# Kernel tuning notes

Measured on AMD Instinct MI355X. Metric: run time of the kernel, lower is better.

## Reference

```python
import jax, jax.numpy as jnp
import numpy as np

B, T, H, W = 1, 8, 48, 48
EMBED, HEADS = 512, 8
HD = EMBED // HEADS          # 64
KS = 3                       # spatial neighborhood kernel
ROT = HD // 3                # 21 -> 2*(21//2)=20 rotary dims per axis, 60 total
MAX_FREQ = 256.0
EPS = 1e-6


def _rms_norm(x, w):
    return x * jax.lax.rsqrt(jnp.mean(x * x, axis=-1, keepdims=True) + EPS) * w


def _axis_freqs(L, base):
    # freqs_for='pixel': positions in [-1, 1], freqs = linspace(1, max_freq/2)*pi
    pos = jnp.linspace(-1.0, 1.0, L)
    f = pos[:, None] * base[None, :]          # (L, ROT//2)
    return jnp.repeat(f, 2, axis=-1)          # (L, 2*(ROT//2)) interleaved pairs


def _axial_freqs(t, h, w):
    base = jnp.linspace(1.0, MAX_FREQ / 2.0, ROT // 2) * jnp.pi
    ft, fh, fw = _axis_freqs(t, base), _axis_freqs(h, base), _axis_freqs(w, base)
    d = ft.shape[-1]
    ft = jnp.broadcast_to(ft[:, None, None, :], (t, h, w, d))
    fh = jnp.broadcast_to(fh[None, :, None, :], (t, h, w, d))
    fw = jnp.broadcast_to(fw[None, None, :, :], (t, h, w, d))
    return jnp.concatenate([ft, fh, fw], axis=-1)  # (t, h, w, 3*d)


def _rotate_half(x):
    x1, x2 = x[..., ::2], x[..., 1::2]
    return jnp.stack((-x2, x1), axis=-1).reshape(x.shape)


def _apply_rope(freqs, x):
    r = freqs.shape[-1]
    xr, xt = x[..., :r], x[..., r:]
    xr = xr * jnp.cos(freqs) + _rotate_half(xr) * jnp.sin(freqs)
    return jnp.concatenate([xr, xt], axis=-1)


def reference(x, w_qkv, w_out, qnorm_w, knorm_w):
    b, t, h, w, c = x.shape
    # fused QKV: per-head contiguous [q|k|v] chunk of size 3*HD (matches
    # rearrange '(heads head_dim)' with head_dim = 3*HD, then tensor_split(3, -1))
    qkv = (x @ w_qkv.T).reshape(b, t, h, w, HEADS, 3 * HD)
    q, k, v = qkv[..., :HD], qkv[..., HD:2 * HD], qkv[..., 2 * HD:]
    q = _rms_norm(q, qnorm_w)
    k = _rms_norm(k, knorm_w)
    freqs = _axial_freqs(t, h, w)[:, :, :, None, :]  # broadcast over heads
    q = _apply_rope(freqs, q)
    k = _apply_rope(freqs, k)
    # neighborhood attention: full along t, clamped KSxKS window over (h, w)
    ih = jnp.clip(jnp.arange(h) - KS // 2, 0, h - KS)[:, None] + jnp.arange(KS)
    iw = jnp.clip(jnp.arange(w) - KS // 2, 0, w - KS)[:, None] + jnp.arange(KS)
    IH = ih[:, :, None, None]  # (h, KS, 1, 1)
    IW = iw[None, None, :, :]  # (1, 1, w, KS)
    kw = k[:, :, IH, IW]       # (b, t, h, KS, w, KS, heads, HD)
    vw = v[:, :, IH, IW]
    scores = jnp.einsum('btxynd,bsxiyjnd->bntxysij', q, kw) * (HD ** -0.5)
    attn = jax.nn.softmax(scores.reshape(b, HEADS, t, h, w, -1), axis=-1)
    attn = attn.reshape(scores.shape)
    out = jnp.einsum('bntxysij,bsxiyjnd->btxynd', attn, vw)
    out = out.reshape(b, t, h, w, c)
    return out @ w_out.T


def setup_inputs():
    key = jax.random.key(0)
    k1, k2, k3 = jax.random.split(key, 3)
    x = jax.random.normal(k1, (B, T, H, W, EMBED), jnp.float32)
    w_qkv = jax.random.normal(k2, (3 * EMBED, EMBED), jnp.float32) * 0.02
    w_out = jax.random.normal(k3, (EMBED, EMBED), jnp.float32) * 0.02
    qnorm_w = jnp.ones((HD,), jnp.float32)
    knorm_w = jnp.ones((HD,), jnp.float32)
    return dict(x=x, w_qkv=w_qkv, w_out=w_out, qnorm_w=qnorm_w, knorm_w=knorm_w)
```

## Files before the change

### kernel.cpp

```cpp
#include <hip/hip_runtime.h>
#include <hip/hip_bf16.h>
#include <math.h>

#define TOK 18432
#define EMB 512
#define NH 8
#define HD_ 64
#define HH 48
#define WW 48

typedef __attribute__((ext_vector_type(8))) __bf16 bf16x8;
typedef __attribute__((ext_vector_type(4))) float  f32x4;
typedef __attribute__((ext_vector_type(8))) unsigned short u16x8;

__device__ __forceinline__ ushort f2bf(float x) {
    __hip_bfloat16 b = __float2bfloat16(x);
    return *(ushort*)&b;
}
__device__ __forceinline__ float bf2f(ushort u) {
    __hip_bfloat16 b = *(__hip_bfloat16*)&u;
    return __bfloat162float(b);
}

__device__ __forceinline__ void gload16(const void* g, void* l) {
    __builtin_amdgcn_global_load_lds((const __attribute__((address_space(1))) void*)g,
                                     (__attribute__((address_space(3))) void*)l,
                                     16, 0, 0);
}

__device__ __forceinline__ f32x4 mfma_bf16(bf16x8 a, bf16x8 b, f32x4 c) {
    return __builtin_amdgcn_mfma_f32_16x16x32_bf16(a, b, c, 0, 0, 0);
}

__global__ void fill_tabs(float2* __restrict__ tabs) {
    int idx = blockIdx.x * 256 + threadIdx.x;
    if (idx >= 104 * 10) return;
    int row = idx / 10, j = idx % 10;
    float base = fmaf((float)j, 127.0f / 9.0f, 1.0f) * 3.14159265358979323846f;
    float pos;
    if (row < 8)       pos = fmaf((float)row,        2.0f / 7.0f,  -1.0f);
    else if (row < 56) pos = fmaf((float)(row - 8),  2.0f / 47.0f, -1.0f);
    else               pos = fmaf((float)(row - 56), 2.0f / 47.0f, -1.0f);
    float f = pos * base;
    tabs[idx] = make_float2(cosf(f), sinf(f));
}

__global__ __launch_bounds__(256) void conv_hi(const float* __restrict__ src,
                                               ushort* __restrict__ dst, int n4) {
    int i = blockIdx.x * 256 + threadIdx.x;
    if (i >= n4) return;
    float4 v = ((const float4*)src)[i];
    ushort4 h = {f2bf(v.x), f2bf(v.y), f2bf(v.z), f2bf(v.w)};
    ((ushort4*)dst)[i] = h;
}

__global__ __launch_bounds__(256) void gemm_qkv(const ushort* __restrict__ Ah,
                                                const ushort* __restrict__ Bh,
                                                const float2* __restrict__ tabs,
                                                const float* __restrict__ qnw,
                                                const float* __restrict__ knw,
                                                ushort* __restrict__ qbf,
                                                ushort* __restrict__ kbf,
                                                ushort* __restrict__ vbf) {
    const int K = 512, nM = 12;
    __shared__ __align__(16) char smem[32768];
#define AS_(b) ((ushort*)(smem + (b) * 8192))
#define BS_(b) ((ushort*)(smem + 16384 + (b) * 8192))
    int nwg = gridDim.x;
    int bid = blockIdx.x;
    int cpx = nwg >> 3;
    int swz = (bid & 7) * cpx + (bid >> 3);
    int bm = (swz % nM) * 128, bn = (swz / nM) * 128;
    int tid = threadIdx.x;
    int lane = tid & 63, wave = tid >> 6;
    int wr = wave >> 1, wc = wave & 1;
    int fr = lane & 15, kg = lane >> 4;

    f32x4 acc[4][4];
#pragma unroll
    for (int m = 0; m < 4; ++m)
#pragma unroll
        for (int n = 0; n < 4; ++n) acc[m][n] = (f32x4){0.f, 0.f, 0.f, 0.f};

    auto stage = [&](int buf, int k0) {
#pragma unroll
        for (int it = 0; it < 2; ++it) {
            int f = it * 256 + tid;
            int row = f >> 2, ch = f & 3;
            int sl = ch ^ ((row >> 1) & 3);
            gload16(Ah + (size_t)(bm + row) * K + k0 + sl * 8, AS_(buf) + f * 8);
            gload16(Bh + (size_t)(bn + row) * K + k0 + sl * 8, BS_(buf) + f * 8);
        }
    };

    int nt = K >> 5;
    stage(0, 0);
    __syncthreads();
    int cur = 0;
    int ksw = (kg ^ ((fr >> 1) & 3)) * 8;
    for (int t = 0; t < nt; ++t) {
        if (t + 1 < nt) stage(cur ^ 1, (t + 1) << 5);
        bf16x8 bh[4];
#pragma unroll
        for (int n = 0; n < 4; ++n)
            bh[n] = *(const bf16x8*)&BS_(cur)[(wc * 64 + n * 16 + fr) * 32 + ksw];
#pragma unroll
        for (int m = 0; m < 4; ++m) {
            bf16x8 ah = *(const bf16x8*)&AS_(cur)[(wr * 64 + m * 16 + fr) * 32 + ksw];
#pragma unroll
            for (int n = 0; n < 4; ++n)
                acc[m][n] = mfma_bf16(ah, bh[n], acc[m][n]);
        }
        __syncthreads();
        cur ^= 1;
    }

    int g = (bm >> 6) + wr;
    int type = g % 3;
    int h = g / 3;
    ushort* obuf = (type == 0) ? qbf : (type == 1) ? kbf : vbf;
    float qsc = (type == 0) ? 0.125f : 1.0f;
    float4 wv[4];
    if (type < 2) {
        const float* wptr = type ? knw : qnw;
#pragma unroll
        for (int m = 0; m < 4; ++m)
            wv[m] = *(const float4*)&wptr[m * 16 + kg * 4];
    }
    char* tb = smem + wave * 5120;
    size_t obase = (size_t)h * TOK + bn + wc * 64;

#pragma unroll
    for (int hp = 0; hp < 2; ++hp) {
#pragma unroll
        for (int nn = 0; nn < 2; ++nn) {
            int n = hp * 2 + nn;
            int tk = bn + wc * 64 + n * 16 + fr;
            if (type == 2) {
#pragma unroll
                for (int m = 0; m < 4; ++m) {
                    ushort4 pk = {f2bf(acc[m][n][0]), f2bf(acc[m][n][1]),
                                  f2bf(acc[m][n][2]), f2bf(acc[m][n][3])};
                    *(ushort4*)(tb + (nn * 16 + fr) * 160 + (m * 16 + kg * 4) * 2) = pk;
                }
            } else {
                float s = 0.f;
#pragma unroll
                for (int m = 0; m < 4; ++m)
#pragma unroll
                    for (int i = 0; i < 4; ++i)
                        s = fmaf(acc[m][n][i], acc[m][n][i], s);
                s += __shfl_xor(s, 16);
                s += __shfl_xor(s, 32);
                float inv = rsqrtf(s * (1.0f / 64.0f) + 1e-6f);
                int t = tk / (HH * WW);
                int rem = tk % (HH * WW);
                int xx = rem / WW, yy = rem % WW;
#pragma unroll
                for (int m = 0; m < 4; ++m) {
                    float r[4];
                    const float* wm = (const float*)&wv[m];
#pragma unroll
                    for (int u = 0; u < 2; ++u) {
                        int dc0 = m * 16 + kg * 4 + 2 * u;
                        float xn0 = acc[m][n][2 * u]     * inv * wm[2 * u];
                        float xn1 = acc[m][n][2 * u + 1] * inv * wm[2 * u + 1];
                        if (dc0 < 60) {
                            int p = dc0 >> 1;
                            int tr = (p < 10) ? t * 10 + p
                                   : (p < 20) ? (8 + xx) * 10 + (p - 10)
                                              : (56 + yy) * 10 + (p - 20);
                            float2 cs = tabs[tr];
                            r[2 * u]     = fmaf(xn0, cs.x, -xn1 * cs.y);
                            r[2 * u + 1] = fmaf(xn1, cs.x,  xn0 * cs.y);
                        } else {
                            r[2 * u] = xn0;
                            r[2 * u + 1] = xn1;
                        }
                    }
                    ushort4 pk = {f2bf(r[0] * qsc), f2bf(r[1] * qsc),
                                  f2bf(r[2] * qsc), f2bf(r[3] * qsc)};
                    *(ushort4*)(tb + (nn * 16 + fr) * 160 + (m * 16 + kg * 4) * 2) = pk;
                }
            }
        }
#pragma unroll
        for (int j = 0; j < 4; ++j) {
            int row = j * 8 + (lane >> 3);
            int c16 = (lane & 7) * 16;
            u16x8 v = *(const u16x8*)(tb + row * 160 + c16);
            size_t tok = obase + hp * 32 + row;
            *(u16x8*)(obuf + tok * 64 + (lane & 7) * 8) = v;
        }
    }
#undef AS_
#undef BS_
}

__global__ __launch_bounds__(256) void gemm_out(const ushort* __restrict__ Ah,
                                                const ushort* __restrict__ Bh,
                                                float* __restrict__ C) {
    const int N = 512, K = 512, nbx = 4;
    __shared__ __align__(16) ushort As[2][128 * 32];
    __shared__ __align__(16) ushort Bs[2][128 * 32];
    int nwg = gridDim.x;
    int bid = blockIdx.x;
    int cpx = nwg >> 3;
    int swz = (bid & 7) * cpx + (bid >> 3);
    int bm = (swz / nbx) * 128, bn = (swz % nbx) * 128;
    int tid = threadIdx.x;
    int lane = tid & 63, wave = tid >> 6;
    int wr = wave >> 1, wc = wave & 1;
    int fr = lane & 15, kg = lane >> 4;

    f32x4 acc[4][4];
#pragma unroll
    for (int m = 0; m < 4; ++m)
#pragma unroll
        for (int n = 0; n < 4; ++n) acc[m][n] = (f32x4){0.f, 0.f, 0.f, 0.f};

    auto stage = [&](int buf, int k0) {
#pragma unroll
        for (int it = 0; it < 2; ++it) {
            int f = it * 256 + tid;
            int row = f >> 2, ch = f & 3;
            int sl = ch ^ ((row >> 1) & 3);
            gload16(Ah + (size_t)(bm + row) * K + k0 + sl * 8, &As[buf][f * 8]);
            gload16(Bh + (size_t)(bn + row) * K + k0 + sl * 8, &Bs[buf][f * 8]);
        }
    };

    int nt = K >> 5;
    stage(0, 0);
    __syncthreads();
    int cur = 0;
    int ksw = (kg ^ ((fr >> 1) & 3)) * 8;
    for (int t = 0; t < nt; ++t) {
        if (t + 1 < nt) stage(cur ^ 1, (t + 1) << 5);
        bf16x8 bh[4];
#pragma unroll
        for (int n = 0; n < 4; ++n)
            bh[n] = *(const bf16x8*)&Bs[cur][(wc * 64 + n * 16 + fr) * 32 + ksw];
#pragma unroll
        for (int m = 0; m < 4; ++m) {
            bf16x8 ah = *(const bf16x8*)&As[cur][(wr * 64 + m * 16 + fr) * 32 + ksw];
#pragma unroll
            for (int n = 0; n < 4; ++n)
                acc[m][n] = mfma_bf16(ah, bh[n], acc[m][n]);
        }
        __syncthreads();
        cur ^= 1;
    }
#pragma unroll
    for (int m = 0; m < 4; ++m) {
        int row0 = bm + wr * 64 + m * 16 + kg * 4;
#pragma unroll
        for (int n = 0; n < 4; ++n) {
            int col = bn + wc * 64 + n * 16 + fr;
#pragma unroll
            for (int i = 0; i < 4; ++i)
                C[(size_t)(row0 + i) * N + col] = acc[m][n][i];
        }
    }
}

__global__ __launch_bounds__(256) void attn_mfma(const ushort* __restrict__ qbf,
                                                 const ushort* __restrict__ kbf,
                                                 const ushort* __restrict__ vbf,
                                                 ushort* __restrict__ ohi) {
    __shared__ __align__(16) char smem[45056];
    constexpr int Q_OFF = 0;
    constexpr int K_OFF = 4096;
    constexpr int V_OFF = 20480;
    constexpr int P_OFF = 36864;

    int patch = blockIdx.x, head = blockIdx.y;
    int bi = patch / 24, bj = patch % 24;
    int x0 = bi * 2, y0 = bj * 2;
    int ubx = min(max(x0 - 1, 0), 44), uby = min(max(y0 - 1, 0), 44);
    int tid = threadIdx.x, lane = tid & 63, w = tid >> 6;
    int fr = lane & 15, kg = lane >> 4;
    size_t hbase = (size_t)head * TOK;

    {
        int f = tid;
        int row = f >> 3, sp = f & 7, sl = sp ^ (row & 7);
        int t = row >> 2, px = (row >> 1) & 1, py = row & 1;
        size_t tok = ((size_t)(t * HH + x0 + px)) * WW + (y0 + py);
        gload16(qbf + (hbase + tok) * 64 + sl * 8, smem + Q_OFF + f * 16);
    }
#pragma unroll
    for (int it = 0; it < 4; ++it) {
        int f = it * 256 + tid;
        int row = f >> 3, sp = f & 7, sl = sp ^ (row & 7);
        int s = row >> 4, ki = (row >> 2) & 3, kj = row & 3;
        size_t tok = ((size_t)(s * HH + ubx + ki)) * WW + (uby + kj);
        gload16(kbf + (hbase + tok) * 64 + sl * 8, smem + K_OFF + f * 16);
    }
#pragma unroll
    for (int it = 0; it < 2; ++it) {
        int u = it * 256 + tid;
        int sk = u >> 4, dg = u & 15;
        int s = sk >> 2, ki = sk & 3;
        ushort4 rv[4];
#pragma unroll
        for (int kj = 0; kj < 4; ++kj) {
            size_t tok = ((size_t)(s * HH + ubx + ki)) * WW + (uby + kj);
            rv[kj] = *(const ushort4*)(vbf + (hbase + tok) * 64 + dg * 4);
        }
        const ushort* rr = (const ushort*)rv;
#pragma unroll
        for (int dd = 0; dd < 4; ++dd) {
            int d = dg * 4 + dd;
            ushort4 val = {rr[dd], rr[4 + dd], rr[8 + dd], rr[12 + dd]};
            *(ushort4*)(smem + V_OFF + d * 256 + ((sk * 2 * 4) ^ ((d & 7) << 4))) = val;
        }
    }
    __syncthreads();

    if (w < 2) {
        int q = w * 16 + fr;
        bf16x8 qb[2];
#pragma unroll
        for (int ks = 0; ks < 2; ++ks)
            qb[ks] = *(const bf16x8*)(smem + Q_OFF + q * 128 +
                                      ((ks * 64 + kg * 16) ^ ((fr & 7) << 4)));
        f32x4 sc[8];
#pragma unroll
        for (int m = 0; m < 8; ++m) sc[m] = (f32x4){0.f, 0.f, 0.f, 0.f};
#pragma unroll
        for (int m = 0; m < 8; ++m)
#pragma unroll
            for (int ks = 0; ks < 2; ++ks) {
                bf16x8 a = *(const bf16x8*)(smem + K_OFF + (m * 16 + fr) * 128 +
                                            ((ks * 64 + kg * 16) ^ ((fr & 7) << 4)));
                sc[m] = mfma_bf16(a, qb[ks], sc[m]);
            }
        int xq = x0 + ((q >> 1) & 1), yq = y0 + (q & 1);
        int lox = min(max(xq - 1, 0), 45) - ubx;
        int loy = min(max(yq - 1, 0), 45) - uby;
        bool vki = ((unsigned)(kg - lox)) <= 2u;
        float mx = -1e30f;
        if (vki) {
#pragma unroll
            for (int m = 0; m < 8; ++m)
#pragma unroll
                for (int i = 0; i < 4; ++i)
                    if (((unsigned)(i - loy)) <= 2u) mx = fmaxf(mx, sc[m][i]);
        }
        mx = fmaxf(mx, __shfl_xor(mx, 16));
        mx = fmaxf(mx, __shfl_xor(mx, 32));
        float sum = 0.f;
#pragma unroll
        for (int m = 0; m < 8; ++m)
#pragma unroll
            for (int i = 0; i < 4; ++i) {
                bool v = vki && (((unsigned)(i - loy)) <= 2u);
                float e = v ? __expf(sc[m][i] - mx) : 0.f;
                sc[m][i] = e;
                sum += e;
            }
        sum += __shfl_xor(sum, 16);
        sum += __shfl_xor(sum, 32);
        float inv = 1.0f / sum;
#pragma unroll
        for (int m = 0; m < 8; ++m) {
            ushort4 pk = {f2bf(sc[m][0] * inv), f2bf(sc[m][1] * inv),
                          f2bf(sc[m][2] * inv), f2bf(sc[m][3] * inv)};
            *(ushort4*)(smem + P_OFF + q * 256 +
                        ((m * 32 + kg * 8) ^ ((q & 7) << 4))) = pk;
        }
    }
    __syncthreads();

    f32x4 ov[2];
    ov[0] = (f32x4){0.f, 0.f, 0.f, 0.f};
    ov[1] = (f32x4){0.f, 0.f, 0.f, 0.f};
#pragma unroll
    for (int kb = 0; kb < 4; ++kb) {
        bf16x8 a = *(const bf16x8*)(smem + V_OFF + (w * 16 + fr) * 256 +
                                    ((kb * 64 + kg * 16) ^ ((fr & 7) << 4)));
#pragma unroll
        for (int nt2 = 0; nt2 < 2; ++nt2) {
            bf16x8 b = *(const bf16x8*)(smem + P_OFF + (nt2 * 16 + fr) * 256 +
                                        ((kb * 64 + kg * 16) ^ ((fr & 7) << 4)));
            ov[nt2] = mfma_bf16(a, b, ov[nt2]);
        }
    }
#pragma unroll
    for (int nt2 = 0; nt2 < 2; ++nt2) {
        int q = nt2 * 16 + fr;
        int t = q >> 2, px = (q >> 1) & 1, py = q & 1;
        size_t tok = ((size_t)(t * HH + x0 + px)) * WW + (y0 + py);
        size_t ob = tok * 512 + head * 64 + w * 16 + kg * 4;
        ushort4 hv = {f2bf(ov[nt2][0]), f2bf(ov[nt2][1]),
                      f2bf(ov[nt2][2]), f2bf(ov[nt2][3])};
        *(ushort4*)&ohi[ob] = hv;
    }
}

extern "C" void kernel_launch(void* const* d_in, const int* in_sizes, int n_in,
                              void* d_out, int out_size, void* d_ws, size_t ws_size,
                              hipStream_t stream) {
    const float* x     = (const float*)d_in[0];
    const float* w_qkv = (const float*)d_in[1];
    const float* w_out = (const float*)d_in[2];
    const float* qnw   = (const float*)d_in[3];
    const float* knw   = (const float*)d_in[4];
    float* out = (float*)d_out;
    char*  ws  = (char*)d_ws;

    const size_t TABS_B = 16384;
    const size_t WQ_B   = (size_t)1536 * 512 * 2;
    const size_t WO_B   = (size_t)512 * 512 * 2;

    float2* tabs = (float2*)ws;
    ushort* wqhi = (ushort*)(ws + TABS_B);
    ushort* wohi = wqhi + (size_t)1536 * 512;
    ushort* qbf  = (ushort*)(ws + TABS_B + WQ_B + WO_B);
    ushort* kbf  = qbf + (size_t)TOK * 512;
    ushort* vbf  = kbf + (size_t)TOK * 512;
    ushort* ohi  = vbf + (size_t)TOK * 512;

    ushort* xhi = (ushort*)d_out;

    fill_tabs<<<5, 256, 0, stream>>>(tabs);
    conv_hi<<<(TOK * 512 / 4 + 255) / 256, 256, 0, stream>>>(x, xhi, TOK * 512 / 4);
    conv_hi<<<(1536 * 512 / 4 + 255) / 256, 256, 0, stream>>>(w_qkv, wqhi, 1536 * 512 / 4);
    conv_hi<<<(512 * 512 / 4 + 255) / 256, 256, 0, stream>>>(w_out, wohi, 512 * 512 / 4);

    gemm_qkv<<<(1536 / 128) * (TOK / 128), 256, 0, stream>>>(
        wqhi, xhi, tabs, qnw, knw, qbf, kbf, vbf);
    attn_mfma<<<dim3(576, NH), 256, 0, stream>>>(qbf, kbf, vbf, ohi);
    gemm_out<<<(TOK / 128) * (512 / 128), 256, 0, stream>>>(ohi, wohi, out);
}
```

Baseline: 117.2 us.

## Fuse x fp32-to-bf16 conversion into QKV GEMM staging and merge init kernels

The separate pass that converted x to bf16 is removed. The QKV GEMM now loads fp32 x tiles straight into registers, converts them, and writes them to LDS while the MFMAs run, instead of using a direct global-to-LDS copy of pre-converted data. The two weight conversions and the rope table fill are merged into one launch. This saves a full read and write of x plus several launches, but each x tile is now re-read in fp32 by all 12 N-blocks, which doubles that traffic, and the B staging goes through registers.

```diff
diff --git a/kernel.cpp b/kernel.cpp
--- a/kernel.cpp
+++ b/kernel.cpp
@@ -32,30 +32,35 @@
     return __builtin_amdgcn_mfma_f32_16x16x32_bf16(a, b, c, 0, 0, 0);
 }
 
-__global__ void fill_tabs(float2* __restrict__ tabs) {
-    int idx = blockIdx.x * 256 + threadIdx.x;
-    if (idx >= 104 * 10) return;
-    int row = idx / 10, j = idx % 10;
-    float base = fmaf((float)j, 127.0f / 9.0f, 1.0f) * 3.14159265358979323846f;
-    float pos;
-    if (row < 8)       pos = fmaf((float)row,        2.0f / 7.0f,  -1.0f);
-    else if (row < 56) pos = fmaf((float)(row - 8),  2.0f / 47.0f, -1.0f);
-    else               pos = fmaf((float)(row - 56), 2.0f / 47.0f, -1.0f);
-    float f = pos * base;
-    tabs[idx] = make_float2(cosf(f), sinf(f));
-}
-
-__global__ __launch_bounds__(256) void conv_hi(const float* __restrict__ src,
-                                               ushort* __restrict__ dst, int n4) {
-    int i = blockIdx.x * 256 + threadIdx.x;
-    if (i >= n4) return;
-    float4 v = ((const float4*)src)[i];
-    ushort4 h = {f2bf(v.x), f2bf(v.y), f2bf(v.z), f2bf(v.w)};
-    ((ushort4*)dst)[i] = h;
+__global__ __launch_bounds__(256) void init_misc(const float* __restrict__ wq,
+                                                 ushort* __restrict__ wqhi,
+                                                 const float* __restrict__ wo,
+                                                 ushort* __restrict__ wohi,
+                                                 float2* __restrict__ tabs) {
+    int b = blockIdx.x;
+    if (b < 1024) {
+        const float* src = (b < 768) ? wq : wo;
+        ushort* dst = (b < 768) ? wqhi : wohi;
+        int i = (b < 768 ? b : b - 768) * 256 + threadIdx.x;
+        float4 v = ((const float4*)src)[i];
+        ushort4 h = {f2bf(v.x), f2bf(v.y), f2bf(v.z), f2bf(v.w)};
+        ((ushort4*)dst)[i] = h;
+    } else {
+        int idx = (b - 1024) * 256 + threadIdx.x;
+        if (idx >= 104 * 10) return;
+        int row = idx / 10, j = idx % 10;
+        float base = fmaf((float)j, 127.0f / 9.0f, 1.0f) * 3.14159265358979323846f;
+        float pos;
+        if (row < 8)       pos = fmaf((float)row,        2.0f / 7.0f,  -1.0f);
+        else if (row < 56) pos = fmaf((float)(row - 8),  2.0f / 47.0f, -1.0f);
+        else               pos = fmaf((float)(row - 56), 2.0f / 47.0f, -1.0f);
+        float f = pos * base;
+        tabs[idx] = make_float2(cosf(f), sinf(f));
+    }
 }
 
 __global__ __launch_bounds__(256) void gemm_qkv(const ushort* __restrict__ Ah,
-                                                const ushort* __restrict__ Bh,
+                                                const float* __restrict__ Bx,
                                                 const float2* __restrict__ tabs,
                                                 const float* __restrict__ qnw,
                                                 const float* __restrict__ knw,
@@ -82,24 +87,46 @@
 #pragma unroll
         for (int n = 0; n < 4; ++n) acc[m][n] = (f32x4){0.f, 0.f, 0.f, 0.f};
 
-    auto stage = [&](int buf, int k0) {
-#pragma unroll
-        for (int it = 0; it < 2; ++it) {
-            int f = it * 256 + tid;
-            int row = f >> 2, ch = f & 3;
-            int sl = ch ^ ((row >> 1) & 3);
-            gload16(Ah + (size_t)(bm + row) * K + k0 + sl * 8, AS_(buf) + f * 8);
-            gload16(Bh + (size_t)(bn + row) * K + k0 + sl * 8, BS_(buf) + f * 8);
-        }
+    int rowA0 = tid >> 2,           chA0 = tid & 3;
+    int slA0 = chA0 ^ ((rowA0 >> 1) & 3);
+    int rowA1 = (256 + tid) >> 2,   chA1 = (256 + tid) & 3;
+    int slA1 = chA1 ^ ((rowA1 >> 1) & 3);
+    const float* bsrc0 = Bx + (size_t)(bn + rowA0) * K + slA0 * 8;
+    const float* bsrc1 = Bx + (size_t)(bn + rowA1) * K + slA1 * 8;
+
+    auto issueA = [&](int buf, int k0) {
+        gload16(Ah + (size_t)(bm + rowA0) * K + k0 + slA0 * 8, AS_(buf) + tid * 8);
+        gload16(Ah + (size_t)(bm + rowA1) * K + k0 + slA1 * 8, AS_(buf) + (256 + tid) * 8);
     };
 
     int nt = K >> 5;
-    stage(0, 0);
+    issueA(0, 0);
+    {
+        float4 b00 = *(const float4*)(bsrc0);
+        float4 b01 = *(const float4*)(bsrc0 + 4);
+        float4 b10 = *(const float4*)(bsrc1);
+        float4 b11 = *(const float4*)(bsrc1 + 4);
+        u16x8 w0 = {f2bf(b00.x), f2bf(b00.y), f2bf(b00.z), f2bf(b00.w),
+                    f2bf(b01.x), f2bf(b01.y), f2bf(b01.z), f2bf(b01.w)};
+        u16x8 w1 = {f2bf(b10.x), f2bf(b10.y), f2bf(b10.z), f2bf(b10.w),
+                    f2bf(b11.x), f2bf(b11.y), f2bf(b11.z), f2bf(b11.w)};
+        *(u16x8*)(BS_(0) + tid * 8) = w0;
+        *(u16x8*)(BS_(0) + (256 + tid) * 8) = w1;
+    }
     __syncthreads();
+
     int cur = 0;
     int ksw = (kg ^ ((fr >> 1) & 3)) * 8;
     for (int t = 0; t < nt; ++t) {
-        if (t + 1 < nt) stage(cur ^ 1, (t + 1) << 5);
+        float4 b00, b01, b10, b11;
+        if (t + 1 < nt) {
+            int k0n = (t + 1) << 5;
+            issueA(cur ^ 1, k0n);
+            b00 = *(const float4*)(bsrc0 + k0n);
+            b01 = *(const float4*)(bsrc0 + k0n + 4);
+            b10 = *(const float4*)(bsrc1 + k0n);
+            b11 = *(const float4*)(bsrc1 + k0n + 4);
+        }
         bf16x8 bh[4];
 #pragma unroll
         for (int n = 0; n < 4; ++n)
@@ -110,6 +137,14 @@
 #pragma unroll
             for (int n = 0; n < 4; ++n)
                 acc[m][n] = mfma_bf16(ah, bh[n], acc[m][n]);
+        }
+        if (t + 1 < nt) {
+            u16x8 w0 = {f2bf(b00.x), f2bf(b00.y), f2bf(b00.z), f2bf(b00.w),
+                        f2bf(b01.x), f2bf(b01.y), f2bf(b01.z), f2bf(b01.w)};
+            u16x8 w1 = {f2bf(b10.x), f2bf(b10.y), f2bf(b10.z), f2bf(b10.w),
+                        f2bf(b11.x), f2bf(b11.y), f2bf(b11.z), f2bf(b11.w)};
+            *(u16x8*)(BS_(cur ^ 1) + tid * 8) = w0;
+            *(u16x8*)(BS_(cur ^ 1) + (256 + tid) * 8) = w1;
         }
         __syncthreads();
         cur ^= 1;
@@ -313,7 +348,7 @@
         for (int dd = 0; dd < 4; ++dd) {
             int d = dg * 4 + dd;
             ushort4 val = {rr[dd], rr[4 + dd], rr[8 + dd], rr[12 + dd]};
-            *(ushort4*)(smem + V_OFF + d * 256 + ((sk * 2 * 4) ^ ((d & 7) << 4))) = val;
+            *(ushort4*)(smem + V_OFF + d * 256 + ((sk * 8) ^ ((d & 7) << 4))) = val;
         }
     }
     __syncthreads();
@@ -422,15 +457,10 @@
     ushort* vbf  = kbf + (size_t)TOK * 512;
     ushort* ohi  = vbf + (size_t)TOK * 512;
 
-    ushort* xhi = (ushort*)d_out;
-
-    fill_tabs<<<5, 256, 0, stream>>>(tabs);
-    conv_hi<<<(TOK * 512 / 4 + 255) / 256, 256, 0, stream>>>(x, xhi, TOK * 512 / 4);
-    conv_hi<<<(1536 * 512 / 4 + 255) / 256, 256, 0, stream>>>(w_qkv, wqhi, 1536 * 512 / 4);
-    conv_hi<<<(512 * 512 / 4 + 255) / 256, 256, 0, stream>>>(w_out, wohi, 512 * 512 / 4);
+    init_misc<<<1029, 256, 0, stream>>>(w_qkv, wqhi, w_out, wohi, tabs);
 
     gemm_qkv<<<(1536 / 128) * (TOK / 128), 256, 0, stream>>>(
-        wqhi, xhi, tabs, qnw, knw, qbf, kbf, vbf);
+        wqhi, x, tabs, qnw, knw, qbf, kbf, vbf);
     attn_mfma<<<dim3(576, NH), 256, 0, stream>>>(qbf, kbf, vbf, ohi);
     gemm_out<<<(TOK / 128) * (512 / 128), 256, 0, stream>>>(ohi, wohi, out);
 }
```

Result: faster. 113.1 us (-3.5%).

## Fuse x fp32-to-bf16 conversion into QKV GEMM and merge init kernels

Applied to the files above, without the earlier changes.

The separate pass that converts the activation tensor x to bf16 is removed. The QKV GEMM now stages fp32 x tiles directly into LDS with a swizzled layout and converts them to bf16 while loading MFMA fragments. The weight conversions and the rotary table fill are merged into a single launch. This saves a full read and write of x and several launches. In exchange it doubles the LDS footprint and B-tile load traffic per GEMM block, and it repeats the conversion work for each of the 12 M-tiles that read the same x tile.

```diff
diff --git a/kernel.cpp b/kernel.cpp
--- a/kernel.cpp
+++ b/kernel.cpp
@@ -32,30 +32,35 @@
     return __builtin_amdgcn_mfma_f32_16x16x32_bf16(a, b, c, 0, 0, 0);
 }
 
-__global__ void fill_tabs(float2* __restrict__ tabs) {
-    int idx = blockIdx.x * 256 + threadIdx.x;
-    if (idx >= 104 * 10) return;
-    int row = idx / 10, j = idx % 10;
-    float base = fmaf((float)j, 127.0f / 9.0f, 1.0f) * 3.14159265358979323846f;
-    float pos;
-    if (row < 8)       pos = fmaf((float)row,        2.0f / 7.0f,  -1.0f);
-    else if (row < 56) pos = fmaf((float)(row - 8),  2.0f / 47.0f, -1.0f);
-    else               pos = fmaf((float)(row - 56), 2.0f / 47.0f, -1.0f);
-    float f = pos * base;
-    tabs[idx] = make_float2(cosf(f), sinf(f));
-}
-
-__global__ __launch_bounds__(256) void conv_hi(const float* __restrict__ src,
-                                               ushort* __restrict__ dst, int n4) {
-    int i = blockIdx.x * 256 + threadIdx.x;
-    if (i >= n4) return;
-    float4 v = ((const float4*)src)[i];
-    ushort4 h = {f2bf(v.x), f2bf(v.y), f2bf(v.z), f2bf(v.w)};
-    ((ushort4*)dst)[i] = h;
+__global__ __launch_bounds__(256) void init_misc(const float* __restrict__ wq,
+                                                 ushort* __restrict__ wqhi,
+                                                 const float* __restrict__ wo,
+                                                 ushort* __restrict__ wohi,
+                                                 float2* __restrict__ tabs) {
+    int b = blockIdx.x;
+    if (b < 1024) {
+        const float* src = (b < 768) ? wq : wo;
+        ushort* dst = (b < 768) ? wqhi : wohi;
+        int i = (b < 768 ? b : b - 768) * 256 + threadIdx.x;
+        float4 v = ((const float4*)src)[i];
+        ushort4 h = {f2bf(v.x), f2bf(v.y), f2bf(v.z), f2bf(v.w)};
+        ((ushort4*)dst)[i] = h;
+    } else {
+        int idx = (b - 1024) * 256 + threadIdx.x;
+        if (idx >= 104 * 10) return;
+        int row = idx / 10, j = idx % 10;
+        float base = fmaf((float)j, 127.0f / 9.0f, 1.0f) * 3.14159265358979323846f;
+        float pos;
+        if (row < 8)       pos = fmaf((float)row,        2.0f / 7.0f,  -1.0f);
+        else if (row < 56) pos = fmaf((float)(row - 8),  2.0f / 47.0f, -1.0f);
+        else               pos = fmaf((float)(row - 56), 2.0f / 47.0f, -1.0f);
+        float f = pos * base;
+        tabs[idx] = make_float2(cosf(f), sinf(f));
+    }
 }
 
 __global__ __launch_bounds__(256) void gemm_qkv(const ushort* __restrict__ Ah,
-                                                const ushort* __restrict__ Bh,
+                                                const float* __restrict__ Bx,
                                                 const float2* __restrict__ tabs,
                                                 const float* __restrict__ qnw,
                                                 const float* __restrict__ knw,
@@ -63,9 +68,9 @@
                                                 ushort* __restrict__ kbf,
                                                 ushort* __restrict__ vbf) {
     const int K = 512, nM = 12;
-    __shared__ __align__(16) char smem[32768];
-#define AS_(b) ((ushort*)(smem + (b) * 8192))
-#define BS_(b) ((ushort*)(smem + 16384 + (b) * 8192))
+    __shared__ __align__(16) char smem[49152];
+#define AS_(b)  ((ushort*)(smem + (b) * 8192))
+#define BSF_(b) ((float*)(smem + 16384 + (b) * 16384))
     int nwg = gridDim.x;
     int bid = blockIdx.x;
     int cpx = nwg >> 3;
@@ -89,7 +94,13 @@
             int row = f >> 2, ch = f & 3;
             int sl = ch ^ ((row >> 1) & 3);
             gload16(Ah + (size_t)(bm + row) * K + k0 + sl * 8, AS_(buf) + f * 8);
-            gload16(Bh + (size_t)(bn + row) * K + k0 + sl * 8, BS_(buf) + f * 8);
+        }
+#pragma unroll
+        for (int it = 0; it < 4; ++it) {
+            int f = it * 256 + tid;
+            int row = f >> 3, ch = f & 7;
+            int sl = ch ^ (row & 7);
+            gload16(Bx + (size_t)(bn + row) * K + k0 + sl * 4, BSF_(buf) + f * 4);
         }
     };
 
@@ -97,16 +108,24 @@
     stage(0, 0);
     __syncthreads();
     int cur = 0;
-    int ksw = (kg ^ ((fr >> 1) & 3)) * 8;
+    int aw = (kg ^ ((fr >> 1) & 3)) * 8;
+    int r7 = fr & 7;
     for (int t = 0; t < nt; ++t) {
         if (t + 1 < nt) stage(cur ^ 1, (t + 1) << 5);
+        const float* BF = BSF_(cur);
         bf16x8 bh[4];
 #pragma unroll
-        for (int n = 0; n < 4; ++n)
-            bh[n] = *(const bf16x8*)&BS_(cur)[(wc * 64 + n * 16 + fr) * 32 + ksw];
+        for (int n = 0; n < 4; ++n) {
+            int R = wc * 64 + n * 16 + fr;
+            f32x4 lo = *(const f32x4*)(BF + R * 32 + (((kg * 2)     ^ r7) << 2));
+            f32x4 hi = *(const f32x4*)(BF + R * 32 + (((kg * 2 + 1) ^ r7) << 2));
+            u16x8 tw = {f2bf(lo[0]), f2bf(lo[1]), f2bf(lo[2]), f2bf(lo[3]),
+                        f2bf(hi[0]), f2bf(hi[1]), f2bf(hi[2]), f2bf(hi[3])};
+            bh[n] = *(bf16x8*)&tw;
+        }
 #pragma unroll
         for (int m = 0; m < 4; ++m) {
-            bf16x8 ah = *(const bf16x8*)&AS_(cur)[(wr * 64 + m * 16 + fr) * 32 + ksw];
+            bf16x8 ah = *(const bf16x8*)&AS_(cur)[(wr * 64 + m * 16 + fr) * 32 + aw];
 #pragma unroll
             for (int n = 0; n < 4; ++n)
                 acc[m][n] = mfma_bf16(ah, bh[n], acc[m][n]);
@@ -194,7 +213,7 @@
         }
     }
 #undef AS_
-#undef BS_
+#undef BSF_
 }
 
 __global__ __launch_bounds__(256) void gemm_out(const ushort* __restrict__ Ah,
@@ -313,7 +332,7 @@
         for (int dd = 0; dd < 4; ++dd) {
             int d = dg * 4 + dd;
             ushort4 val = {rr[dd], rr[4 + dd], rr[8 + dd], rr[12 + dd]};
-            *(ushort4*)(smem + V_OFF + d * 256 + ((sk * 2 * 4) ^ ((d & 7) << 4))) = val;
+            *(ushort4*)(smem + V_OFF + d * 256 + ((sk * 8) ^ ((d & 7) << 4))) = val;
         }
     }
     __syncthreads();
@@ -422,15 +441,10 @@
     ushort* vbf  = kbf + (size_t)TOK * 512;
     ushort* ohi  = vbf + (size_t)TOK * 512;
 
-    ushort* xhi = (ushort*)d_out;
-
-    fill_tabs<<<5, 256, 0, stream>>>(tabs);
-    conv_hi<<<(TOK * 512 / 4 + 255) / 256, 256, 0, stream>>>(x, xhi, TOK * 512 / 4);
-    conv_hi<<<(1536 * 512 / 4 + 255) / 256, 256, 0, stream>>>(w_qkv, wqhi, 1536 * 512 / 4);
-    conv_hi<<<(512 * 512 / 4 + 255) / 256, 256, 0, stream>>>(w_out, wohi, 512 * 512 / 4);
+    init_misc<<<1029, 256, 0, stream>>>(w_qkv, wqhi, w_out, wohi, tabs);
 
     gemm_qkv<<<(1536 / 128) * (TOK / 128), 256, 0, stream>>>(
-        wqhi, xhi, tabs, qnw, knw, qbf, kbf, vbf);
+        wqhi, x, tabs, qnw, knw, qbf, kbf, vbf);
     attn_mfma<<<dim3(576, NH), 256, 0, stream>>>(qbf, kbf, vbf, ohi);
     gemm_out<<<(TOK / 128) * (512 / 128), 256, 0, stream>>>(ohi, wohi, out);
 }
```

Result: no change. 115.1 us (-1.8%).

## Triple-buffer GEMM staging with vmcnt waits and merge conversion kernels

Applied to the files above, without the earlier changes.

Both GEMMs move from double to triple LDS buffering. Each iteration waits only on the older loads via s_waitcnt vmcnt(4) and uses a single raw barrier instead of two __syncthreads, which lets the next tile load overlap compute. Separately, the three bf16 conversion kernels and the rope table fill are merged into one launch to cut launch overhead. The cost is 48KB of LDS per block, which may lower occupancy, and the hand-written waitcnt counts depend on how many loads the compiler emits per stage.

```diff
diff --git a/kernel.cpp b/kernel.cpp
--- a/kernel.cpp
+++ b/kernel.cpp
@@ -32,26 +32,36 @@
     return __builtin_amdgcn_mfma_f32_16x16x32_bf16(a, b, c, 0, 0, 0);
 }
 
-__global__ void fill_tabs(float2* __restrict__ tabs) {
-    int idx = blockIdx.x * 256 + threadIdx.x;
-    if (idx >= 104 * 10) return;
-    int row = idx / 10, j = idx % 10;
-    float base = fmaf((float)j, 127.0f / 9.0f, 1.0f) * 3.14159265358979323846f;
-    float pos;
-    if (row < 8)       pos = fmaf((float)row,        2.0f / 7.0f,  -1.0f);
-    else if (row < 56) pos = fmaf((float)(row - 8),  2.0f / 47.0f, -1.0f);
-    else               pos = fmaf((float)(row - 56), 2.0f / 47.0f, -1.0f);
-    float f = pos * base;
-    tabs[idx] = make_float2(cosf(f), sinf(f));
-}
-
-__global__ __launch_bounds__(256) void conv_hi(const float* __restrict__ src,
-                                               ushort* __restrict__ dst, int n4) {
-    int i = blockIdx.x * 256 + threadIdx.x;
-    if (i >= n4) return;
-    float4 v = ((const float4*)src)[i];
-    ushort4 h = {f2bf(v.x), f2bf(v.y), f2bf(v.z), f2bf(v.w)};
-    ((ushort4*)dst)[i] = h;
+__global__ __launch_bounds__(256) void init_misc(const float* __restrict__ x,
+                                                 ushort* __restrict__ xhi,
+                                                 const float* __restrict__ wq,
+                                                 ushort* __restrict__ wqhi,
+                                                 const float* __restrict__ wo,
+                                                 ushort* __restrict__ wohi,
+                                                 float2* __restrict__ tabs) {
+    int b = blockIdx.x;
+    if (b < 10240) {
+        const float* src;
+        ushort* dst;
+        int i;
+        if (b < 9216)      { src = x;  dst = xhi;  i = b * 256 + threadIdx.x; }
+        else if (b < 9984) { src = wq; dst = wqhi; i = (b - 9216) * 256 + threadIdx.x; }
+        else               { src = wo; dst = wohi; i = (b - 9984) * 256 + threadIdx.x; }
+        float4 v = ((const float4*)src)[i];
+        ushort4 h = {f2bf(v.x), f2bf(v.y), f2bf(v.z), f2bf(v.w)};
+        ((ushort4*)dst)[i] = h;
+    } else {
+        int idx = (b - 10240) * 256 + threadIdx.x;
+        if (idx >= 104 * 10) return;
+        int row = idx / 10, j = idx % 10;
+        float base = fmaf((float)j, 127.0f / 9.0f, 1.0f) * 3.14159265358979323846f;
+        float pos;
+        if (row < 8)       pos = fmaf((float)row,        2.0f / 7.0f,  -1.0f);
+        else if (row < 56) pos = fmaf((float)(row - 8),  2.0f / 47.0f, -1.0f);
+        else               pos = fmaf((float)(row - 56), 2.0f / 47.0f, -1.0f);
+        float f = pos * base;
+        tabs[idx] = make_float2(cosf(f), sinf(f));
+    }
 }
 
 __global__ __launch_bounds__(256) void gemm_qkv(const ushort* __restrict__ Ah,
@@ -63,9 +73,9 @@
                                                 ushort* __restrict__ kbf,
                                                 ushort* __restrict__ vbf) {
     const int K = 512, nM = 12;
-    __shared__ __align__(16) char smem[32768];
-#define AS_(b) ((ushort*)(smem + (b) * 8192))
-#define BS_(b) ((ushort*)(smem + 16384 + (b) * 8192))
+    __shared__ __align__(16) char smem[49152];
+#define AS_(b) ((ushort*)(smem + (b) * 16384))
+#define BS_(b) ((ushort*)(smem + (b) * 16384 + 8192))
     int nwg = gridDim.x;
     int bid = blockIdx.x;
     int cpx = nwg >> 3;
@@ -95,25 +105,34 @@
 
     int nt = K >> 5;
     stage(0, 0);
-    __syncthreads();
-    int cur = 0;
+    int cb = 0, nb = 1;
     int ksw = (kg ^ ((fr >> 1) & 3)) * 8;
     for (int t = 0; t < nt; ++t) {
-        if (t + 1 < nt) stage(cur ^ 1, (t + 1) << 5);
+        if (t + 1 < nt) {
+            stage(nb, (t + 1) << 5);
+            asm volatile("s_waitcnt vmcnt(4)" ::: "memory");
+        } else {
+            asm volatile("s_waitcnt vmcnt(0)" ::: "memory");
+        }
+        __builtin_amdgcn_s_barrier();
+        __builtin_amdgcn_sched_barrier(0);
+        const ushort* Bc = BS_(cb);
+        const ushort* Ac = AS_(cb);
         bf16x8 bh[4];
 #pragma unroll
         for (int n = 0; n < 4; ++n)
-            bh[n] = *(const bf16x8*)&BS_(cur)[(wc * 64 + n * 16 + fr) * 32 + ksw];
+            bh[n] = *(const bf16x8*)&Bc[(wc * 64 + n * 16 + fr) * 32 + ksw];
 #pragma unroll
         for (int m = 0; m < 4; ++m) {
-            bf16x8 ah = *(const bf16x8*)&AS_(cur)[(wr * 64 + m * 16 + fr) * 32 + ksw];
+            bf16x8 ah = *(const bf16x8*)&Ac[(wr * 64 + m * 16 + fr) * 32 + ksw];
 #pragma unroll
             for (int n = 0; n < 4; ++n)
                 acc[m][n] = mfma_bf16(ah, bh[n], acc[m][n]);
         }
-        __syncthreads();
-        cur ^= 1;
-    }
+        cb = (cb + 1 == 3) ? 0 : cb + 1;
+        nb = (nb + 1 == 3) ? 0 : nb + 1;
+    }
+    __syncthreads();
 
     int g = (bm >> 6) + wr;
     int type = g % 3;
@@ -201,8 +220,9 @@
                                                 const ushort* __restrict__ Bh,
                                                 float* __restrict__ C) {
     const int N = 512, K = 512, nbx = 4;
-    __shared__ __align__(16) ushort As[2][128 * 32];
-    __shared__ __align__(16) ushort Bs[2][128 * 32];
+    __shared__ __align__(16) char smem[49152];
+#define AS_(b) ((ushort*)(smem + (b) * 16384))
+#define BS_(b) ((ushort*)(smem + (b) * 16384 + 8192))
     int nwg = gridDim.x;
     int bid = blockIdx.x;
     int cpx = nwg >> 3;
@@ -225,31 +245,39 @@
             int f = it * 256 + tid;
             int row = f >> 2, ch = f & 3;
             int sl = ch ^ ((row >> 1) & 3);
-            gload16(Ah + (size_t)(bm + row) * K + k0 + sl * 8, &As[buf][f * 8]);
-            gload16(Bh + (size_t)(bn + row) * K + k0 + sl * 8, &Bs[buf][f * 8]);
+            gload16(Ah + (size_t)(bm + row) * K + k0 + sl * 8, AS_(buf) + f * 8);
+            gload16(Bh + (size_t)(bn + row) * K + k0 + sl * 8, BS_(buf) + f * 8);
         }
     };
 
     int nt = K >> 5;
     stage(0, 0);
-    __syncthreads();
-    int cur = 0;
+    int cb = 0, nb = 1;
     int ksw = (kg ^ ((fr >> 1) & 3)) * 8;
     for (int t = 0; t < nt; ++t) {
-        if (t + 1 < nt) stage(cur ^ 1, (t + 1) << 5);
+        if (t + 1 < nt) {
+            stage(nb, (t + 1) << 5);
+            asm volatile("s_waitcnt vmcnt(4)" ::: "memory");
+        } else {
+            asm volatile("s_waitcnt vmcnt(0)" ::: "memory");
+        }
+        __builtin_amdgcn_s_barrier();
+        __builtin_amdgcn_sched_barrier(0);
+        const ushort* Bc = BS_(cb);
+        const ushort* Ac = AS_(cb);
         bf16x8 bh[4];
 #pragma unroll
         for (int n = 0; n < 4; ++n)
-            bh[n] = *(const bf16x8*)&Bs[cur][(wc * 64 + n * 16 + fr) * 32 + ksw];
+            bh[n] = *(const bf16x8*)&Bc[(wc * 64 + n * 16 + fr) * 32 + ksw];
 #pragma unroll
         for (int m = 0; m < 4; ++m) {
-            bf16x8 ah = *(const bf16x8*)&As[cur][(wr * 64 + m * 16 + fr) * 32 + ksw];
+            bf16x8 ah = *(const bf16x8*)&Ac[(wr * 64 + m * 16 + fr) * 32 + ksw];
 #pragma unroll
             for (int n = 0; n < 4; ++n)
                 acc[m][n] = mfma_bf16(ah, bh[n], acc[m][n]);
         }
-        __syncthreads();
-        cur ^= 1;
+        cb = (cb + 1 == 3) ? 0 : cb + 1;
+        nb = (nb + 1 == 3) ? 0 : nb + 1;
     }
 #pragma unroll
     for (int m = 0; m < 4; ++m) {
@@ -262,6 +290,8 @@
                 C[(size_t)(row0 + i) * N + col] = acc[m][n][i];
         }
     }
+#undef AS_
+#undef BS_
 }
 
 __global__ __launch_bounds__(256) void attn_mfma(const ushort* __restrict__ qbf,
@@ -313,7 +343,7 @@
         for (int dd = 0; dd < 4; ++dd) {
             int d = dg * 4 + dd;
             ushort4 val = {rr[dd], rr[4 + dd], rr[8 + dd], rr[12 + dd]};
-            *(ushort4*)(smem + V_OFF + d * 256 + ((sk * 2 * 4) ^ ((d & 7) << 4))) = val;
+            *(ushort4*)(smem + V_OFF + d * 256 + ((sk * 8) ^ ((d & 7) << 4))) = val;
         }
     }
     __syncthreads();
@@ -424,10 +454,7 @@
 
     ushort* xhi = (ushort*)d_out;
 
-    fill_tabs<<<5, 256, 0, stream>>>(tabs);
-    conv_hi<<<(TOK * 512 / 4 + 255) / 256, 256, 0, stream>>>(x, xhi, TOK * 512 / 4);
-    conv_hi<<<(1536 * 512 / 4 + 255) / 256, 256, 0, stream>>>(w_qkv, wqhi, 1536 * 512 / 4);
-    conv_hi<<<(512 * 512 / 4 + 255) / 256, 256, 0, stream>>>(w_out, wohi, 512 * 512 / 4);
+    init_misc<<<10245, 256, 0, stream>>>(x, xhi, w_qkv, wqhi, w_out, wohi, tabs);
 
     gemm_qkv<<<(1536 / 128) * (TOK / 128), 256, 0, stream>>>(
         wqhi, xhi, tabs, qnw, knw, qbf, kbf, vbf);
```

New measurement: 104.4 us. 11.0% less time.
